# Optimization experiments

Hardware: AMD Instinct MI355X
Metric: run time of the kernel (lower is better)

## Reference

```python
import jax, jax.numpy as jnp
import numpy as np

D = 2048  # input_dimensions (== seq_len, required by the module's math)
H = 8192  # hidden_dimensions
B = 4
S = D


def setup_inputs() -> dict:
    key = jax.random.key(0)
    ks = jax.random.split(key, 13)
    scale_in = 1.0 / np.sqrt(D)
    scale_hid = 1.0 / np.sqrt(H)
    def lin(k, fan_in, fan_out, s):
        return jax.random.normal(k, (fan_in, fan_out), jnp.float32) * s
    inp = {"x": jax.random.normal(ks[0], (B, S, D), jnp.float32)}
    names = ["q", "k", "v"]
    for i, n in enumerate(names):
        inp[f"{n}_w1"] = lin(ks[1 + 4 * i], D, H, scale_in)
        inp[f"{n}_b1"] = jnp.zeros((H,), jnp.float32)
        inp[f"{n}_w2"] = lin(ks[2 + 4 * i], H, D, scale_hid)
        inp[f"{n}_b2"] = jnp.zeros((D,), jnp.float32)
    return inp


def _mlp(x, w1, b1, w2, b2):
    # Linear(D,H) -> ReLU -> Linear(H,D)
    h = jax.nn.relu(jnp.einsum("bsd,dh->bsh", x, w1) + b1)
    return jnp.einsum("bsh,hd->bsd", h, w2) + b2


def reference(x, q_w1, q_b1, q_w2, q_b2, k_w1, k_b1, k_w2, k_b2,
              v_w1, v_b1, v_w2, v_b2):
    Q = _mlp(x, q_w1, q_b1, q_w2, q_b2)
    K = _mlp(x, k_w1, k_b1, k_w2, k_b2)
    V = _mlp(x, v_w1, v_b1, v_w2, v_b2)
    # scores: Q @ K^T  -> [B, S, S]  (no 1/sqrt(d) scaling in original)
    scores = jnp.einsum("bsd,btd->bst", Q, K)
    # nn.Softmax(dim=1): over axis 1 (rows), NOT the usual last axis
    probs = jax.nn.softmax(scores, axis=1)
    # original computes V @ probs (requires S == D)
    out = jnp.einsum("bsd,bdt->bst", V, probs)
    return out
```

## Files before the change

### kernel.cpp

```cpp
#include <hip/hip_runtime.h>
#include <cstdint>
#include <cstddef>

typedef __attribute__((ext_vector_type(8))) short short8;
typedef __attribute__((ext_vector_type(4))) short short4v;
typedef __attribute__((ext_vector_type(4))) float f32x4;
typedef __attribute__((ext_vector_type(4))) int i32x4;

#define DEV __device__ __forceinline__

constexpr int DD = 2048;
constexpr int HHID = 8192;
constexpr int BB = 4;
constexpr int SS = 2048;
constexpr size_t NX = (size_t)BB * SS * DD;
constexpr size_t NW = (size_t)DD * HHID;
constexpr size_t NH = (size_t)BB * SS * HHID;

constexpr size_t OFF_XH  = 0;
constexpr size_t OFF_XA1 = OFF_XH + NX * 2;
constexpr size_t OFF_XA2 = OFF_XA1 + NX;
constexpr size_t OFF_WA1 = OFF_XA2 + NX;
constexpr size_t OFF_WA2 = OFF_WA1 + NW;
constexpr size_t OFF_WHV = OFF_WA1;
constexpr size_t OFF_HH  = OFF_WA2 + NW;
constexpr size_t OFF_HL  = OFF_HH + NH * 2;
constexpr size_t OFF_QKH = OFF_HL + NH * 2;
constexpr size_t OFF_QKL = OFF_QKH + NX * 2;
constexpr size_t OFF_QA1 = OFF_QKL + NX * 2;
constexpr size_t OFF_QA2 = OFF_QA1 + NX;
constexpr size_t OFF_KA1 = OFF_QA2 + NX;
constexpr size_t OFF_KA2 = OFF_KA1 + NX;
constexpr size_t OFF_HA1 = OFF_KA2 + NX;
constexpr size_t OFF_HA2 = OFF_HA1 + NH;
constexpr size_t OFF_V   = OFF_HA2 + NH;
constexpr size_t OFF_XS  = OFF_V + NX * 2;
constexpr size_t OFF_HS  = OFF_XS + 32768;
constexpr size_t OFF_QS  = OFF_HS + 32768;
constexpr size_t OFF_KS  = OFF_QS + 32768;
constexpr size_t OFF_CM  = OFF_KS + 32768;
constexpr size_t WS_TOTAL = OFF_CM + 32768;
constexpr size_t OFF_ST = OFF_HH;
constexpr size_t OFF_PT = OFF_HL;

__device__ __align__(256) unsigned char g_ws[WS_TOTAL];

DEV unsigned char* wsbase(unsigned char* p) { return p ? p : (unsigned char*)g_ws; }
DEV short f2bf(float v) { __bf16 b = (__bf16)v; return __builtin_bit_cast(short, b); }
DEV float bf2f(short s) { return (float)__builtin_bit_cast(__bf16, s); }

template <typename T> DEV void nts(T v, T* p) { __builtin_nontemporal_store(v, p); }
template <typename T> DEV T ntl(const T* p) { return __builtin_nontemporal_load(p); }

DEV void gl16(const short* g, short* l) {
  __builtin_amdgcn_global_load_lds((const __attribute__((address_space(1))) void*)g,
                                   (__attribute__((address_space(3))) void*)l, 16, 0, 0);
}
DEV void gl16b(const signed char* g, signed char* l) {
  __builtin_amdgcn_global_load_lds((const __attribute__((address_space(1))) void*)g,
                                   (__attribute__((address_space(3))) void*)l, 16, 0, 0);
}

DEV void raster2d(int rem, int gx, int grp, int& by, int& bx) {
  const int tpg = grp * gx;
  const int gidx = rem / tpg;
  const int o = rem - gidx * tpg;
  const int r = o / grp;
  by = gidx * grp + (o - r * grp);
  bx = r;
}

__global__ void cast_hi_k(const float* __restrict__ x, unsigned char* wsb,
                          size_t oh, size_t n4) {
  unsigned char* ws = wsbase(wsb);
  short4v* OH = (short4v*)(ws + oh);
  const f32x4* X = (const f32x4*)x;
  for (size_t i = (size_t)blockIdx.x * blockDim.x + threadIdx.x; i < n4;
       i += (size_t)gridDim.x * blockDim.x) {
    const f32x4 v = ntl(&X[i]);
    short4v hs;
#pragma unroll
    for (int e = 0; e < 4; ++e) hs[e] = f2bf(v[e]);
    OH[i] = hs;
  }
}

__launch_bounds__(256)
__global__ void quant_x_k(const float* __restrict__ x, unsigned char* wsb,
                          size_t oa1, size_t oa2, size_t oxs) {
  unsigned char* ws = wsbase(wsb);
  signed char* A1 = (signed char*)(ws + oa1);
  signed char* A2 = (signed char*)(ws + oa2);
  float* XS = (float*)(ws + oxs);
  const int row = blockIdx.x;
  const float* xr = x + (size_t)row * 2048;
  const int tid = threadIdx.x, lane = tid & 63;
  const f32x4 v0 = *(const f32x4*)&xr[tid * 8];
  const f32x4 v1 = *(const f32x4*)&xr[tid * 8 + 4];
  float m = 0.0f;
#pragma unroll
  for (int e = 0; e < 4; ++e) m = fmaxf(m, fmaxf(fabsf(v0[e]), fabsf(v1[e])));
#pragma unroll
  for (int o = 32; o; o >>= 1) m = fmaxf(m, __shfl_xor(m, o));
  __shared__ float rb[4];
  if (lane == 0) rb[tid >> 6] = m;
  __syncthreads();
  m = fmaxf(fmaxf(rb[0], rb[1]), fmaxf(rb[2], rb[3]));
  const float inv = (m > 1e-30f) ? 127.0f / m : 0.0f;
  if (tid == 0) XS[row] = m * (1.0f / 127.0f);
  unsigned int w1a = 0, w1b = 0, w2a = 0, w2b = 0;
#pragma unroll
  for (int e = 0; e < 8; ++e) {
    const float xv = (e < 4) ? v0[e] : v1[e - 4];
    const float q = xv * inv;
    const float a1f = rintf(q);
    int ia2 = (int)rintf((q - a1f) * 256.0f);
    ia2 = ia2 > 127 ? 127 : (ia2 < -127 ? -127 : ia2);
    const unsigned int b1 = (unsigned char)(signed char)(int)a1f;
    const unsigned int b2 = (unsigned char)(signed char)ia2;
    if (e < 4) { w1a |= b1 << (8 * e); w2a |= b2 << (8 * e); }
    else       { w1b |= b1 << (8 * (e - 4)); w2b |= b2 << (8 * (e - 4)); }
  }
  const size_t o = (size_t)row * 2048 + tid * 8;
  *(unsigned int*)&A1[o] = w1a; *(unsigned int*)&A1[o + 4] = w1b;
  *(unsigned int*)&A2[o] = w2a; *(unsigned int*)&A2[o + 4] = w2b;
}

__launch_bounds__(1024)
__global__ void rowquant_k(unsigned char* wsb, size_t hho, size_t hlo,
                           size_t oa1, size_t oa2, size_t oso, int rowlen) {
  unsigned char* ws = wsbase(wsb);
  const int row = blockIdx.x, tid = threadIdx.x, lane = tid & 63, wv = tid >> 6;
  const int nw = blockDim.x >> 6;
  const short8 hi = ntl((const short8*)((const short*)(ws + hho) + (size_t)row * rowlen) + tid);
  const short8 lo = ntl((const short8*)((const short*)(ws + hlo) + (size_t)row * rowlen) + tid);
  float v[8]; float m = 0.0f;
#pragma unroll
  for (int e = 0; e < 8; ++e) {
    v[e] = bf2f(hi[e]) + bf2f(lo[e]);
    m = fmaxf(m, fabsf(v[e]));
  }
#pragma unroll
  for (int o = 32; o; o >>= 1) m = fmaxf(m, __shfl_xor(m, o));
  __shared__ float rb[16];
  if (lane == 0) rb[wv] = m;
  __syncthreads();
  m = rb[0];
  for (int i = 1; i < nw; ++i) m = fmaxf(m, rb[i]);
  const float inv = (m > 1e-30f) ? 127.0f / m : 0.0f;
  if (tid == 0) ((float*)(ws + oso))[row] = m * (1.0f / 127.0f);
  unsigned int w1a = 0, w1b = 0, w2a = 0, w2b = 0;
#pragma unroll
  for (int e = 0; e < 8; ++e) {
    const float q = v[e] * inv;
    const float a1f = rintf(q);
    int ia2 = (int)rintf((q - a1f) * 256.0f);
    ia2 = ia2 > 127 ? 127 : (ia2 < -127 ? -127 : ia2);
    const unsigned int b1 = (unsigned char)(signed char)(int)a1f;
    const unsigned int b2 = (unsigned char)(signed char)ia2;
    if (e < 4) { w1a |= b1 << (8 * e); w2a |= b2 << (8 * e); }
    else       { w1b |= b1 << (8 * (e - 4)); w2b |= b2 << (8 * (e - 4)); }
  }
  const size_t o = (size_t)row * rowlen + tid * 8;
  signed char* A1 = (signed char*)(ws + oa1);
  signed char* A2 = (signed char*)(ws + oa2);
  *(unsigned int*)&A1[o] = w1a; *(unsigned int*)&A1[o + 4] = w1b;
  *(unsigned int*)&A2[o] = w2a; *(unsigned int*)&A2[o + 4] = w2b;
}

__launch_bounds__(256)
__global__ void colmax_k(const float* __restrict__ w, unsigned char* wsb,
                         size_t omax, int R, int C) {
  unsigned char* ws = wsbase(wsb);
  unsigned int* MX = (unsigned int*)(ws + omax);
  const int col = blockIdx.x * 256 + threadIdx.x;
  const int r0 = blockIdx.y * 128;
  float m = 0.0f;
  for (int r = 0; r < 128; ++r) m = fmaxf(m, fabsf(w[(size_t)(r0 + r) * C + col]));
  atomicMax(&MX[col], __float_as_uint(m));
}

__global__ void scalefix_k(unsigned char* wsb, size_t off, int n) {
  unsigned char* ws = wsbase(wsb);
  const int i = blockIdx.x * 256 + threadIdx.x;
  if (i < n) {
    float* p = (float*)(ws + off);
    const unsigned int u = ((const unsigned int*)p)[i];
    p[i] = __uint_as_float(u) * (1.0f / 127.0f);
  }
}

__global__ void transpose_quant_k(const float* __restrict__ src, unsigned char* wsb,
                                  size_t oa1, size_t oa2, size_t osc, int R, int C) {
  __shared__ float t[32][33];
  unsigned char* ws = wsbase(wsb);
  signed char* A1 = (signed char*)(ws + oa1);
  signed char* A2 = (signed char*)(ws + oa2);
  const float* SC = (const float*)(ws + osc);
  const int c0 = blockIdx.x << 5, r0 = blockIdx.y << 5;
  const int x = threadIdx.x, y = threadIdx.y;
#pragma unroll
  for (int i = 0; i < 4; ++i) {
    const int rr = y + (i << 3);
    t[rr][x] = ntl(&src[(size_t)(r0 + rr) * C + c0 + x]);
  }
  __syncthreads();
#pragma unroll
  for (int i = 0; i < 4; ++i) {
    const int oc = y + (i << 3);
    const float v = t[x][oc];
    const float s = SC[c0 + oc];
    const float inv = (s > 1e-38f) ? 1.0f / s : 0.0f;
    const float q = v * inv;
    const float a1f = rintf(q);
    int ia2 = (int)rintf((q - a1f) * 256.0f);
    ia2 = ia2 > 127 ? 127 : (ia2 < -127 ? -127 : ia2);
    const size_t o = (size_t)(c0 + oc) * R + r0 + x;
    A1[o] = (signed char)(int)a1f;
    A2[o] = (signed char)ia2;
  }
}

__global__ void transpose_cast_k(const float* __restrict__ src, unsigned char* wsb,
                                 size_t oh, int R, int C) {
  __shared__ float t[32][33];
  unsigned char* ws = wsbase(wsb);
  short* OH = (short*)(ws + oh);
  const int c0 = blockIdx.x << 5, r0 = blockIdx.y << 5;
  const int x = threadIdx.x, y = threadIdx.y;
#pragma unroll
  for (int i = 0; i < 4; ++i) {
    const int rr = y + (i << 3);
    t[rr][x] = ntl(&src[(size_t)(r0 + rr) * C + c0 + x]);
  }
  __syncthreads();
#pragma unroll
  for (int i = 0; i < 4; ++i) {
    const int oc = y + (i << 3);
    OH[(size_t)(c0 + oc) * R + r0 + x] = f2bf(t[x][oc]);
  }
}

DEV i32x4 mfma_i8(i32x4 a, i32x4 b, i32x4 c) {
  return __builtin_amdgcn_mfma_i32_16x16x64_i8(a, b, c, 0, 0, 0);
}
DEV i32x4 rfi8(const signed char* base, int lstride, int L, int row, int fg) {
  return *(const i32x4*)&base[L * lstride + row * 64 + ((fg ^ ((row >> 1) & 3)) << 4)];
}

template <bool RELU, int STORE>
__launch_bounds__(512, 2)
__global__ void gemm_i8_k(unsigned char* wsb,
                          size_t a1o, size_t a2o, size_t b1o, size_t b2o,
                          size_t aso, size_t bso, const float* __restrict__ bias,
                          size_t o0, size_t o1, int M, int N, int K,
                          int gx, int gxy, int grp) {
  __shared__ alignas(16) signed char lds8[114688];

  unsigned char* ws = wsbase(wsb);
  const int tid = threadIdx.x;
  const int lane = tid & 63;
  const int wave = tid >> 6;
  const int wm = (wave >> 2) << 6;
  const int wn = (wave & 3) << 6;
  const int fr = lane & 15;
  const int fg = lane >> 4;

  const int nwg = gridDim.x;
  const int q8 = nwg >> 3;
  const int id = (blockIdx.x & 7) * q8 + (blockIdx.x >> 3);
  const int bz = id / gxy;
  const int rem = id - bz * gxy;
  int by, bx;
  raster2d(rem, gx, grp, by, bx);
  const int brow = by << 7;
  const int bcol = bx << 8;

  const size_t batchA = (size_t)bz * M * K;
  const size_t batchB = (STORE == 2) ? (size_t)bz * N * K : 0;
  const signed char* Xa1 = (const signed char*)(ws + a1o) + batchA;
  const signed char* Xa2 = (const signed char*)(ws + a2o) + batchA;
  const signed char* Wa1 = (const signed char*)(ws + b1o) + batchB;
  const signed char* Wa2 = (const signed char*)(ws + b2o) + batchB;
  const float* AS = (const float*)(ws + aso) + (size_t)bz * M;
  const float* BS = (const float*)(ws + bso) + ((STORE == 2) ? (size_t)bz * N : 0);

  const int ar = tid >> 2, ac = tid & 3;
  const size_t aOff = (size_t)(brow + ar) * K + ((ac ^ ((ar >> 1) & 3)) << 4);
  size_t bOff[2];
#pragma unroll
  for (int h = 0; h < 2; ++h) {
    const int G = tid + h * 512;
    const int r = G >> 2, c = G & 3;
    bOff[h] = (size_t)(bcol + r) * K + ((c ^ ((r >> 1) & 3)) << 4);
  }

  auto stageA = [&](int slotBase, int tt) {
    const int ko = tt * 64;
    gl16b(Xa1 + aOff + ko, &lds8[slotBase + (tid << 4)]);
    gl16b(Xa2 + aOff + ko, &lds8[slotBase + 8192 + (tid << 4)]);
  };
  auto stageB = [&](int slotBase, int tt) {
    const int ko = tt * 64;
#pragma unroll
    for (int h = 0; h < 2; ++h) {
      gl16b(Wa1 + bOff[h] + ko, &lds8[slotBase + ((tid + h * 512) << 4)]);
      gl16b(Wa2 + bOff[h] + ko, &lds8[slotBase + 16384 + ((tid + h * 512) << 4)]);
    }
  };

  const int nt = K / 64;
  i32x4 I1[4][4] = {};
  i32x4 I2[4][4] = {};

  stageA(0, 0);
  stageB(49152, 0);
  if (nt > 1) { stageA(16384, 1); stageB(49152 + 32768, 1); }
  if (nt > 1) { asm volatile("s_waitcnt vmcnt(6)" ::: "memory"); }
  else        { asm volatile("s_waitcnt vmcnt(0)" ::: "memory"); }
  __builtin_amdgcn_s_barrier();

  for (int t = 0; t < nt; ++t) {
    const signed char* aS = &lds8[(t % 3) * 16384];
    const signed char* bS = &lds8[49152 + (t & 1) * 32768];
    const int sA2 = ((t + 2) % 3) * 16384;
    const int sB2 = 49152 + (t & 1) * 32768;
    const bool pf = (t + 2 < nt);
    i32x4 bf[4][2], af[2][2];

    if (pf) stageA(sA2, t + 2);
#pragma unroll
    for (int j = 0; j < 4; ++j) {
      bf[j][0] = rfi8(bS, 16384, 0, wn + j * 16 + fr, fg);
      bf[j][1] = rfi8(bS, 16384, 1, wn + j * 16 + fr, fg);
    }
#pragma unroll
    for (int i = 0; i < 2; ++i) {
      af[i][0] = rfi8(aS, 8192, 0, wm + i * 16 + fr, fg);
      af[i][1] = rfi8(aS, 8192, 1, wm + i * 16 + fr, fg);
    }
    __builtin_amdgcn_s_setprio(1);
#pragma unroll
    for (int i = 0; i < 2; ++i)
#pragma unroll
      for (int j = 0; j < 4; ++j) {
        I1[i][j] = mfma_i8(af[i][0], bf[j][0], I1[i][j]);
        I2[i][j] = mfma_i8(af[i][0], bf[j][1], I2[i][j]);
        I2[i][j] = mfma_i8(af[i][1], bf[j][0], I2[i][j]);
      }
    __builtin_amdgcn_s_setprio(0);
    __builtin_amdgcn_s_barrier();

    asm volatile("" ::: "memory");
    if (pf) stageB(sB2, t + 2);
#pragma unroll
    for (int i = 0; i < 2; ++i) {
      af[i][0] = rfi8(aS, 8192, 0, wm + (2 + i) * 16 + fr, fg);
      af[i][1] = rfi8(aS, 8192, 1, wm + (2 + i) * 16 + fr, fg);
    }
    __builtin_amdgcn_s_setprio(1);
#pragma unroll
    for (int i = 0; i < 2; ++i)
#pragma unroll
      for (int j = 0; j < 4; ++j) {
        I1[2 + i][j] = mfma_i8(af[i][0], bf[j][0], I1[2 + i][j]);
        I2[2 + i][j] = mfma_i8(af[i][0], bf[j][1], I2[2 + i][j]);
        I2[2 + i][j] = mfma_i8(af[i][1], bf[j][0], I2[2 + i][j]);
      }
    __builtin_amdgcn_s_setprio(0);
    if (pf) { asm volatile("s_waitcnt vmcnt(6)" ::: "memory"); }
    else    { asm volatile("s_waitcnt vmcnt(0)" ::: "memory"); }
    __builtin_amdgcn_s_barrier();
  }

  const int fq4 = fg << 2;
  if constexpr (STORE == 0) {
    short* ldsS = (short*)lds8;
    short* Oh = (short*)(ws + o0);
    short* Ol = (short*)(ws + o1);
#pragma unroll
    for (int rd = 0; rd < 2; ++rd) {
      __builtin_amdgcn_s_barrier();
#pragma unroll
      for (int i = 0; i < 4; ++i) {
        const int rl = wm + i * 16 + fq4;
        const f32x4 sa4 = *(const f32x4*)&AS[brow + rl];
#pragma unroll
        for (int j = 0; j < 4; ++j) {
          const int cl = wn + j * 16 + fr;
          const float sb = BS[bcol + cl];
          const float bv = bias ? bias[bcol + cl] : 0.0f;
#pragma unroll
          for (int e = 0; e < 4; ++e) {
            float u = ((float)I1[i][j][e] + (float)I2[i][j][e] * (1.0f / 256.0f)) *
                          (sa4[e] * sb) + bv;
            if (RELU) u = fmaxf(u, 0.0f);
            short v;
            if (rd == 0) {
              v = f2bf(u);
            } else {
              const short hb = f2bf(u);
              v = f2bf(u - bf2f(hb));
            }
            ldsS[(rl + e) * 264 + cl] = v;
          }
        }
      }
      __builtin_amdgcn_s_barrier();
      short* gout = (rd == 0) ? Oh : Ol;
#pragma unroll
      for (int gi = 0; gi < 8; ++gi) {
        const int g = gi * 512 + tid;
        const int row = g >> 5, cg = g & 31;
        const short8 v = *(const short8*)&ldsS[row * 264 + cg * 8];
        nts(v, (short8*)&gout[(size_t)(brow + row) * N + bcol + cg * 8]);
      }
    }
  } else {
    float* Of = (float*)(ws + o0) + (size_t)bz * M * N;
    float* ldsf = (float*)lds8;
#pragma unroll
    for (int h2 = 0; h2 < 2; ++h2) {
      __builtin_amdgcn_s_barrier();
      if ((wn >> 7) == h2) {
#pragma unroll
        for (int i = 0; i < 4; ++i) {
          const int rl = wm + i * 16 + fq4;
          const f32x4 sa4 = *(const f32x4*)&AS[brow + rl];
#pragma unroll
          for (int j = 0; j < 4; ++j) {
            const int cp = (wn & 127) + j * 16 + fr;
            const float sb = BS[bcol + wn + j * 16 + fr];
            f32x4 u;
#pragma unroll
            for (int e = 0; e < 4; ++e)
              u[e] = ((float)I1[i][j][e] + (float)I2[i][j][e] * (1.0f / 256.0f)) *
                     (sa4[e] * sb);
            *(f32x4*)&ldsf[cp * 132 + rl] = u;
          }
        }
      }
      __builtin_amdgcn_s_barrier();
#pragma unroll
      for (int gi = 0; gi < 8; ++gi) {
        const int g = gi * 512 + tid;
        const int tr = g >> 5, tc4 = (g & 31) << 2;
        const f32x4 v = *(const f32x4*)&ldsf[tr * 132 + tc4];
        nts(v, (f32x4*)&Of[(size_t)(bcol + h2 * 128 + tr) * M + brow + tc4]);
      }
    }
  }
}

constexpr int CH = 8192;

DEV short8 read_frag1(const short* base, int row, int s, int fg) {
  return *(const short8*)&base[row * 64 + ((((s << 2) | fg) ^ (row & 7)) << 3)];
}

DEV f32x4 mfma16(short8 a, short8 b, f32x4 c) {
  return __builtin_amdgcn_mfma_f32_16x16x32_bf16(a, b, c, 0, 0, 0);
}

template <bool RELU, int STORE>
__launch_bounds__(512, 2)
__global__ void gemm8_k(unsigned char* wsb,
                        size_t aoff0, size_t boff0,
                        const float* __restrict__ bias,
                        size_t ooff0, float* __restrict__ optr,
                        int M, int N, int K, int gx, int gxy, int grp) {
  __shared__ alignas(16) short lds[10 * CH];

  unsigned char* ws = wsbase(wsb);
  const int tid = threadIdx.x;
  const int lane = tid & 63;
  const int wave = tid >> 6;
  const int wm = (wave >> 2) << 7;
  const int wn = (wave & 3) << 6;

  const int nwg = gridDim.x;
  const int q8 = nwg >> 3;
  const int id = (blockIdx.x & 7) * q8 + (blockIdx.x >> 3);
  const int bz = id / gxy;
  const int rem = id - bz * gxy;
  int by, bx;
  raster2d(rem, gx, grp, by, bx);
  const int brow = by << 8;
  const int bcol = bx << 8;

  const short* A0 = (const short*)(ws + aoff0) + (size_t)bz * M * K;
  const short* B0g = (const short*)(ws + boff0) + (size_t)bz * N * K;

  size_t aSrc[2][2], bSrc[2][2];
#pragma unroll
  for (int h = 0; h < 2; ++h) {
    const int G = tid + h * 512;
    const int r = G >> 3, c = G & 7;
#pragma unroll
    for (int qq = 0; qq < 2; ++qq) {
      aSrc[qq][h] = (size_t)(brow + qq * 128 + r) * K + (size_t)((c ^ (r & 7)) << 3);
      bSrc[qq][h] = (size_t)(bcol + qq * 128 + r) * K + (size_t)((c ^ (r & 7)) << 3);
    }
  }
  const int ldst0 = tid << 3;

  auto issueA = [&](int slot, int qq, int tt) {
    short* dst = &lds[slot + qq * CH];
    const size_t ka = (size_t)tt * 64;
    gl16(A0 + aSrc[qq][0] + ka, dst + ldst0);
    gl16(A0 + aSrc[qq][1] + ka, dst + ldst0 + CH / 2);
  };
  auto issueB = [&](int slot, int qq, int tt) {
    short* dst = &lds[slot + qq * CH];
    const size_t ka = (size_t)tt * 64;
    gl16(B0g + bSrc[qq][0] + ka, dst + ldst0);
    gl16(B0g + bSrc[qq][1] + ka, dst + ldst0 + CH / 2);
  };

  const int nt = K / 64;
  const int fr = lane & 15;
  const int fg = lane >> 4;

  f32x4 acc[8][4] = {};

  issueA(0, 0, 0); issueA(0, 1, 0);
  issueB(6 * CH, 0, 0); issueB(6 * CH, 1, 0);
  if (nt > 1) {
    issueA(2 * CH, 0, 1); issueA(2 * CH, 1, 1);
    issueB(8 * CH, 0, 1); issueB(8 * CH, 1, 1);
    asm volatile("s_waitcnt vmcnt(8)" ::: "memory");
  } else {
    asm volatile("s_waitcnt vmcnt(0)" ::: "memory");
  }
  __builtin_amdgcn_s_barrier();

  for (int t = 0; t < nt; ++t) {
    const short* aBase = &lds[(t % 3) * (2 * CH)];
    const short* bBase = &lds[6 * CH + (t & 1) * (2 * CH)];
    const int sA2 = ((t + 2) % 3) * (2 * CH);
    const int sB  = 6 * CH + (t & 1) * (2 * CH);
    const bool pf = (t + 2 < nt);
    short8 bfr[4][2], av[4][2];

    if (pf) { issueA(sA2, 0, t + 2); issueA(sA2, 1, t + 2); }
#pragma unroll
    for (int j = 0; j < 4; ++j) {
      bfr[j][0] = read_frag1(bBase, wn + j * 16 + fr, 0, fg);
      bfr[j][1] = read_frag1(bBase, wn + j * 16 + fr, 1, fg);
    }
#pragma unroll
    for (int i = 0; i < 4; ++i) {
      av[i][0] = read_frag1(aBase, wm + i * 16 + fr, 0, fg);
      av[i][1] = read_frag1(aBase, wm + i * 16 + fr, 1, fg);
    }
    __builtin_amdgcn_s_setprio(1);
#pragma unroll
    for (int i = 0; i < 4; ++i)
#pragma unroll
      for (int j = 0; j < 4; ++j) {
        acc[i][j] = mfma16(av[i][0], bfr[j][0], acc[i][j]);
        acc[i][j] = mfma16(av[i][1], bfr[j][1], acc[i][j]);
      }
    __builtin_amdgcn_s_setprio(0);
    __builtin_amdgcn_s_barrier();

    asm volatile("" ::: "memory");
    if (pf) { issueB(sB, 0, t + 2); issueB(sB, 1, t + 2); }
#pragma unroll
    for (int i = 0; i < 4; ++i) {
      av[i][0] = read_frag1(aBase, wm + 64 + i * 16 + fr, 0, fg);
      av[i][1] = read_frag1(aBase, wm + 64 + i * 16 + fr, 1, fg);
    }
    __builtin_amdgcn_s_setprio(1);
#pragma unroll
    for (int i = 0; i < 4; ++i)
#pragma unroll
      for (int j = 0; j < 4; ++j) {
        acc[4 + i][j] = mfma16(av[i][0], bfr[j][0], acc[4 + i][j]);
        acc[4 + i][j] = mfma16(av[i][1], bfr[j][1], acc[4 + i][j]);
      }
    __builtin_amdgcn_s_setprio(0);
    if (pf) {
      asm volatile("s_waitcnt vmcnt(8)" ::: "memory");
    } else {
      asm volatile("s_waitcnt vmcnt(0)" ::: "memory");
    }
    __builtin_amdgcn_s_barrier();
  }

  const int fq4 = (lane >> 4) << 2;
  if constexpr (STORE == 1) {
    short* Oh = (short*)(ws + ooff0);
    __builtin_amdgcn_s_barrier();
#pragma unroll
    for (int i = 0; i < 8; ++i) {
      const int rl = wm + i * 16 + fq4;
#pragma unroll
      for (int j = 0; j < 4; ++j) {
        const int cl = wn + j * 16 + fr;
        const float bv = bias ? bias[bcol + cl] : 0.0f;
#pragma unroll
        for (int e = 0; e < 4; ++e) {
          float u = acc[i][j][e] + bv;
          if (RELU) u = fmaxf(u, 0.0f);
          lds[(rl + e) * 264 + cl] = f2bf(u);
        }
      }
    }
    __builtin_amdgcn_s_barrier();
#pragma unroll
    for (int gi = 0; gi < 16; ++gi) {
      const int g = gi * 512 + tid;
      const int row = g >> 5, cg = g & 31;
      const short8 v = *(const short8*)&lds[row * 264 + cg * 8];
      nts(v, (short8*)&Oh[(size_t)(brow + row) * N + bcol + cg * 8]);
    }
  } else {
    float* Op = optr + (size_t)bz * M * N;
    float* ldsf = (float*)lds;
#pragma unroll
    for (int h = 0; h < 2; ++h) {
      __builtin_amdgcn_s_barrier();
      if ((wm & 128) == (h << 7)) {
#pragma unroll
        for (int i = 0; i < 8; ++i) {
          const int rp = (wm & 127) + i * 16 + fq4;
#pragma unroll
          for (int j = 0; j < 4; ++j) {
            const int cl = wn + j * 16 + fr;
#pragma unroll
            for (int e = 0; e < 4; ++e)
              ldsf[(rp + e) * 258 + cl] = acc[i][j][e];
          }
        }
      }
      __builtin_amdgcn_s_barrier();
#pragma unroll
      for (int gi = 0; gi < 16; ++gi) {
        const int g = gi * 512 + tid;
        const int tr = g >> 6, tc4 = (g & 63) << 2;
        const f32x4 v = *(const f32x4*)&ldsf[tr * 258 + tc4];
        nts(v, (f32x4*)&Op[(size_t)(brow + h * 128 + tr) * N + bcol + tc4]);
      }
    }
  }
}

__launch_bounds__(256)
__global__ void softmax_rows_k(unsigned char* wsb, size_t st, size_t pt) {
  constexpr int S = 2048;
  unsigned char* ws = wsbase(wsb);
  const f32x4* row = (const f32x4*)((const float*)(ws + st) + (size_t)blockIdx.x * S);
  short4v* out = (short4v*)((short*)(ws + pt) + (size_t)blockIdx.x * S);
  const int tid = threadIdx.x, lane = tid & 63, wv = tid >> 6;
  const f32x4 a = ntl(&row[tid]);
  const f32x4 b = ntl(&row[tid + 256]);
  float m = fmaxf(fmaxf(fmaxf(a[0], a[1]), fmaxf(a[2], a[3])),
                  fmaxf(fmaxf(b[0], b[1]), fmaxf(b[2], b[3])));
#pragma unroll
  for (int o = 32; o; o >>= 1) m = fmaxf(m, __shfl_xor(m, o));
  __shared__ float rb[8];
  if (lane == 0) rb[wv] = m;
  __syncthreads();
  m = fmaxf(fmaxf(rb[0], rb[1]), fmaxf(rb[2], rb[3]));
  float e[8];
  float s = 0.0f;
#pragma unroll
  for (int q = 0; q < 4; ++q) { e[q] = expf(a[q] - m); s += e[q]; }
#pragma unroll
  for (int q = 0; q < 4; ++q) { e[4 + q] = expf(b[q] - m); s += e[4 + q]; }
#pragma unroll
  for (int o = 32; o; o >>= 1) s += __shfl_xor(s, o);
  if (lane == 0) rb[4 + wv] = s;
  __syncthreads();
  s = rb[4] + rb[5] + rb[6] + rb[7];
  const float inv = 1.0f / s;
  short4v o1, o2;
#pragma unroll
  for (int q = 0; q < 4; ++q) { o1[q] = f2bf(e[q] * inv); o2[q] = f2bf(e[4 + q] * inv); }
  nts(o1, &out[tid]);
  nts(o2, &out[tid + 256]);
}

extern "C" void kernel_launch(void* const* d_in, const int* in_sizes, int n_in,
                              void* d_out, int out_size, void* d_ws, size_t ws_size,
                              hipStream_t stream) {
  const float* x   = (const float*)d_in[0];
  const float* qw1 = (const float*)d_in[1];
  const float* qb1 = (const float*)d_in[2];
  const float* qw2 = (const float*)d_in[3];
  const float* qb2 = (const float*)d_in[4];
  const float* kw1 = (const float*)d_in[5];
  const float* kb1 = (const float*)d_in[6];
  const float* kw2 = (const float*)d_in[7];
  const float* kb2 = (const float*)d_in[8];
  const float* vw1 = (const float*)d_in[9];
  const float* vb1 = (const float*)d_in[10];
  const float* vw2 = (const float*)d_in[11];
  const float* vb2 = (const float*)d_in[12];
  float* out = (float*)d_out;
  unsigned char* wsb = (ws_size >= WS_TOTAL) ? (unsigned char*)d_ws : nullptr;
  unsigned char* wsr;
  if (wsb) wsr = wsb;
  else { hipError_t e = hipGetSymbolAddress((void**)&wsr, HIP_SYMBOL(g_ws)); (void)e; }

  const int M = BB * SS;
  dim3 blk(512);
  dim3 tb(32, 8);

  quant_x_k<<<8192, 256, 0, stream>>>(x, wsb, OFF_XA1, OFF_XA2, OFF_XS);
  cast_hi_k<<<4096, 256, 0, stream>>>(x, wsb, OFF_XH, NX / 4);

  hipMemsetAsync(wsr + OFF_CM, 0, 32768, stream);
  colmax_k<<<dim3(HHID / 256, DD / 128), 256, 0, stream>>>(qw1, wsb, OFF_CM, DD, HHID);
  scalefix_k<<<32, 256, 0, stream>>>(wsb, OFF_CM, HHID);
  transpose_quant_k<<<dim3(HHID / 32, DD / 32), tb, 0, stream>>>(qw1, wsb, OFF_WA1, OFF_WA2, OFF_CM, DD, HHID);
  gemm_i8_k<true, 0><<<2048, blk, 0, stream>>>(wsb, OFF_XA1, OFF_XA2, OFF_WA1, OFF_WA2,
                                               OFF_XS, OFF_CM, qb1, OFF_HH, OFF_HL,
                                               M, HHID, DD, 32, 2048, 8);
  rowquant_k<<<8192, 1024, 0, stream>>>(wsb, OFF_HH, OFF_HL, OFF_HA1, OFF_HA2, OFF_HS, HHID);
  hipMemsetAsync(wsr + OFF_CM, 0, 32768, stream);
  colmax_k<<<dim3(DD / 256, HHID / 128), 256, 0, stream>>>(qw2, wsb, OFF_CM, HHID, DD);
  scalefix_k<<<8, 256, 0, stream>>>(wsb, OFF_CM, DD);
  transpose_quant_k<<<dim3(DD / 32, HHID / 32), tb, 0, stream>>>(qw2, wsb, OFF_WA1, OFF_WA2, OFF_CM, HHID, DD);
  gemm_i8_k<false, 0><<<512, blk, 0, stream>>>(wsb, OFF_HA1, OFF_HA2, OFF_WA1, OFF_WA2,
                                               OFF_HS, OFF_CM, qb2, OFF_QKH, OFF_QKL,
                                               M, DD, HHID, 8, 512, 8);
  rowquant_k<<<8192, 256, 0, stream>>>(wsb, OFF_QKH, OFF_QKL, OFF_QA1, OFF_QA2, OFF_QS, DD);

  hipMemsetAsync(wsr + OFF_CM, 0, 32768, stream);
  colmax_k<<<dim3(HHID / 256, DD / 128), 256, 0, stream>>>(kw1, wsb, OFF_CM, DD, HHID);
  scalefix_k<<<32, 256, 0, stream>>>(wsb, OFF_CM, HHID);
  transpose_quant_k<<<dim3(HHID / 32, DD / 32), tb, 0, stream>>>(kw1, wsb, OFF_WA1, OFF_WA2, OFF_CM, DD, HHID);
  gemm_i8_k<true, 0><<<2048, blk, 0, stream>>>(wsb, OFF_XA1, OFF_XA2, OFF_WA1, OFF_WA2,
                                               OFF_XS, OFF_CM, kb1, OFF_HH, OFF_HL,
                                               M, HHID, DD, 32, 2048, 8);
  rowquant_k<<<8192, 1024, 0, stream>>>(wsb, OFF_HH, OFF_HL, OFF_HA1, OFF_HA2, OFF_HS, HHID);
  hipMemsetAsync(wsr + OFF_CM, 0, 32768, stream);
  colmax_k<<<dim3(DD / 256, HHID / 128), 256, 0, stream>>>(kw2, wsb, OFF_CM, HHID, DD);
  scalefix_k<<<8, 256, 0, stream>>>(wsb, OFF_CM, DD);
  transpose_quant_k<<<dim3(DD / 32, HHID / 32), tb, 0, stream>>>(kw2, wsb, OFF_WA1, OFF_WA2, OFF_CM, HHID, DD);
  gemm_i8_k<false, 0><<<512, blk, 0, stream>>>(wsb, OFF_HA1, OFF_HA2, OFF_WA1, OFF_WA2,
                                               OFF_HS, OFF_CM, kb2, OFF_QKH, OFF_QKL,
                                               M, DD, HHID, 8, 512, 8);
  rowquant_k<<<8192, 256, 0, stream>>>(wsb, OFF_QKH, OFF_QKL, OFF_KA1, OFF_KA2, OFF_KS, DD);

  transpose_cast_k<<<dim3(HHID / 32, DD / 32), tb, 0, stream>>>(vw1, wsb, OFF_WHV, DD, HHID);
  gemm8_k<true, 1><<<1024, blk, 0, stream>>>(
      wsb, OFF_XH, OFF_WHV, vb1, OFF_HH, nullptr, M, HHID, DD, 32, 1024, 4);
  transpose_cast_k<<<dim3(DD / 32, HHID / 32), tb, 0, stream>>>(vw2, wsb, OFF_WHV, HHID, DD);
  gemm8_k<false, 1><<<256, blk, 0, stream>>>(
      wsb, OFF_HH, OFF_WHV, vb2, OFF_V, nullptr, M, DD, HHID, 8, 256, 4);

  gemm_i8_k<false, 2><<<512, blk, 0, stream>>>(wsb, OFF_QA1, OFF_QA2, OFF_KA1, OFF_KA2,
                                               OFF_QS, OFF_KS, nullptr, OFF_ST, 0,
                                               SS, SS, DD, 8, 128, 8);

  softmax_rows_k<<<BB * SS, 256, 0, stream>>>(wsb, OFF_ST, OFF_PT);

  gemm8_k<false, 3><<<256, blk, 0, stream>>>(
      wsb, OFF_V, OFF_PT, nullptr, 0, out, SS, SS, DD, 8, 64, 4);
}
```

Measured before the change: 2.672 ms.

## Fuse int8 row quantization into GEMM epilogue with per-tile scales and rescale pass

The GEMM epilogue now quantizes its output directly to the two-level int8 format, using a per-tile row max, and writes per-tile scales. It no longer writes a bf16 hi/lo pair that a separate row-quantization kernel reread. A light rescale kernel then computes each row's global max and requantizes only the tiles whose scale differs. This cuts the large bf16 intermediate traffic for the hidden and Q/K activations, at the cost of a second rounding step that can lose some precision. Barriers in the epilogues were also switched from raw s_barrier to __syncthreads.

Result: no change. 2.696 ms (+0.9%).

```diff
diff --git a/kernel.cpp b/kernel.cpp
--- a/kernel.cpp
+++ b/kernel.cpp
@@ -24,24 +24,23 @@
 constexpr size_t OFF_WA2 = OFF_WA1 + NW;
 constexpr size_t OFF_WHV = OFF_WA1;
 constexpr size_t OFF_HH  = OFF_WA2 + NW;
-constexpr size_t OFF_HL  = OFF_HH + NH * 2;
-constexpr size_t OFF_QKH = OFF_HL + NH * 2;
-constexpr size_t OFF_QKL = OFF_QKH + NX * 2;
-constexpr size_t OFF_QA1 = OFF_QKL + NX * 2;
+constexpr size_t OFF_PT  = OFF_HH + NH * 2;
+constexpr size_t OFF_HA1 = OFF_PT + NX * 2;
+constexpr size_t OFF_HA2 = OFF_HA1 + NH;
+constexpr size_t OFF_QA1 = OFF_HA2 + NH;
 constexpr size_t OFF_QA2 = OFF_QA1 + NX;
 constexpr size_t OFF_KA1 = OFF_QA2 + NX;
 constexpr size_t OFF_KA2 = OFF_KA1 + NX;
-constexpr size_t OFF_HA1 = OFF_KA2 + NX;
-constexpr size_t OFF_HA2 = OFF_HA1 + NH;
-constexpr size_t OFF_V   = OFF_HA2 + NH;
+constexpr size_t OFF_V   = OFF_KA2 + NX;
 constexpr size_t OFF_XS  = OFF_V + NX * 2;
 constexpr size_t OFF_HS  = OFF_XS + 32768;
 constexpr size_t OFF_QS  = OFF_HS + 32768;
 constexpr size_t OFF_KS  = OFF_QS + 32768;
 constexpr size_t OFF_CM  = OFF_KS + 32768;
-constexpr size_t WS_TOTAL = OFF_CM + 32768;
+constexpr size_t OFF_TSH = OFF_CM + 32768;
+constexpr size_t OFF_TSQ = OFF_TSH + 8192 * 32 * 4;
+constexpr size_t WS_TOTAL = OFF_TSQ + 8192 * 8 * 4;
 constexpr size_t OFF_ST = OFF_HH;
-constexpr size_t OFF_PT = OFF_HL;
 
 __device__ __align__(256) unsigned char g_ws[WS_TOTAL];
 
@@ -126,46 +125,46 @@
   *(unsigned int*)&A2[o] = w2a; *(unsigned int*)&A2[o + 4] = w2b;
 }
 
-__launch_bounds__(1024)
-__global__ void rowquant_k(unsigned char* wsb, size_t hho, size_t hlo,
-                           size_t oa1, size_t oa2, size_t oso, int rowlen) {
-  unsigned char* ws = wsbase(wsb);
-  const int row = blockIdx.x, tid = threadIdx.x, lane = tid & 63, wv = tid >> 6;
-  const int nw = blockDim.x >> 6;
-  const short8 hi = ntl((const short8*)((const short*)(ws + hho) + (size_t)row * rowlen) + tid);
-  const short8 lo = ntl((const short8*)((const short*)(ws + hlo) + (size_t)row * rowlen) + tid);
-  float v[8]; float m = 0.0f;
-#pragma unroll
-  for (int e = 0; e < 8; ++e) {
-    v[e] = bf2f(hi[e]) + bf2f(lo[e]);
-    m = fmaxf(m, fabsf(v[e]));
-  }
-#pragma unroll
-  for (int o = 32; o; o >>= 1) m = fmaxf(m, __shfl_xor(m, o));
-  __shared__ float rb[16];
-  if (lane == 0) rb[wv] = m;
+__launch_bounds__(256)
+__global__ void rescale_k(unsigned char* wsb, size_t a1o, size_t a2o,
+                          size_t tso, size_t so, int rowlen) {
+  unsigned char* ws = wsbase(wsb);
+  const int row = blockIdx.x, tid = threadIdx.x;
+  const int nblk = rowlen >> 8;
+  const float* TS = (const float*)(ws + tso) + (size_t)row * nblk;
+  __shared__ float ratio[32];
+  __shared__ float srow_sh;
+  if (tid == 0) {
+    float m = 0.0f;
+    for (int i = 0; i < nblk; ++i) m = fmaxf(m, TS[i]);
+    srow_sh = m;
+    ((float*)(ws + so))[row] = m;
+  }
   __syncthreads();
-  m = rb[0];
-  for (int i = 1; i < nw; ++i) m = fmaxf(m, rb[i]);
-  const float inv = (m > 1e-30f) ? 127.0f / m : 0.0f;
-  if (tid == 0) ((float*)(ws + oso))[row] = m * (1.0f / 127.0f);
-  unsigned int w1a = 0, w1b = 0, w2a = 0, w2b = 0;
-#pragma unroll
-  for (int e = 0; e < 8; ++e) {
-    const float q = v[e] * inv;
-    const float a1f = rintf(q);
-    int ia2 = (int)rintf((q - a1f) * 256.0f);
-    ia2 = ia2 > 127 ? 127 : (ia2 < -127 ? -127 : ia2);
-    const unsigned int b1 = (unsigned char)(signed char)(int)a1f;
-    const unsigned int b2 = (unsigned char)(signed char)ia2;
-    if (e < 4) { w1a |= b1 << (8 * e); w2a |= b2 << (8 * e); }
-    else       { w1b |= b1 << (8 * (e - 4)); w2b |= b2 << (8 * (e - 4)); }
-  }
-  const size_t o = (size_t)row * rowlen + tid * 8;
-  signed char* A1 = (signed char*)(ws + oa1);
-  signed char* A2 = (signed char*)(ws + oa2);
-  *(unsigned int*)&A1[o] = w1a; *(unsigned int*)&A1[o + 4] = w1b;
-  *(unsigned int*)&A2[o] = w2a; *(unsigned int*)&A2[o + 4] = w2b;
+  const float srow = srow_sh;
+  if (tid < nblk) ratio[tid] = (srow > 0.0f) ? TS[tid] / srow : 0.0f;
+  __syncthreads();
+  unsigned int* A1 = (unsigned int*)((signed char*)(ws + a1o) + (size_t)row * rowlen);
+  unsigned int* A2 = (unsigned int*)((signed char*)(ws + a2o) + (size_t)row * rowlen);
+  const int nu = rowlen >> 2;
+  for (int u = tid; u < nu; u += 256) {
+    const float r = ratio[u >> 6];
+    if (r == 1.0f) continue;
+    const unsigned int w1 = A1[u], w2 = A2[u];
+    unsigned int o1 = 0, o2 = 0;
+#pragma unroll
+    for (int e = 0; e < 4; ++e) {
+      const float a1 = (float)(signed char)(w1 >> (8 * e));
+      const float a2 = (float)(signed char)(w2 >> (8 * e));
+      const float f = r * (a1 + a2 * (1.0f / 256.0f));
+      const float n1 = rintf(f);
+      int i2 = (int)rintf((f - n1) * 256.0f);
+      i2 = i2 > 127 ? 127 : (i2 < -127 ? -127 : i2);
+      o1 |= ((unsigned int)(unsigned char)(signed char)(int)n1) << (8 * e);
+      o2 |= ((unsigned int)(unsigned char)(signed char)i2) << (8 * e);
+    }
+    A1[u] = o1; A2[u] = o2;
+  }
 }
 
 __launch_bounds__(256)
@@ -253,7 +252,7 @@
 __global__ void gemm_i8_k(unsigned char* wsb,
                           size_t a1o, size_t a2o, size_t b1o, size_t b2o,
                           size_t aso, size_t bso, const float* __restrict__ bias,
-                          size_t o0, size_t o1, int M, int N, int K,
+                          size_t o0, size_t o1, size_t o2, int M, int N, int K,
                           int gx, int gxy, int grp) {
   __shared__ alignas(16) signed char lds8[114688];
 
@@ -374,13 +373,54 @@
   }
 
   const int fq4 = fg << 2;
-  if constexpr (STORE == 0) {
-    short* ldsS = (short*)lds8;
-    short* Oh = (short*)(ws + o0);
-    short* Ol = (short*)(ws + o1);
+  if constexpr (STORE == 4) {
+    signed char* O1 = (signed char*)(ws + o0);
+    signed char* O2 = (signed char*)(ws + o1);
+    float* TS = (float*)(ws + o2);
+    const int nblk = N >> 8;
+    unsigned int* rmaxU = (unsigned int*)&lds8[36864];
+    float* rmaxF = (float*)rmaxU;
+    if (tid < 128) rmaxU[tid] = 0;
+    __syncthreads();
+    float sbj[4], bvj[4];
+#pragma unroll
+    for (int j = 0; j < 4; ++j) {
+      const int cl = wn + j * 16 + fr;
+      sbj[j] = BS[bcol + cl];
+      bvj[j] = bias ? bias[bcol + cl] : 0.0f;
+    }
+#pragma unroll
+    for (int i = 0; i < 4; ++i) {
+      const int rl = wm + i * 16 + fq4;
+      const f32x4 sa4 = *(const f32x4*)&AS[brow + rl];
+      float mx[4] = {0.0f, 0.0f, 0.0f, 0.0f};
+#pragma unroll
+      for (int j = 0; j < 4; ++j)
+#pragma unroll
+        for (int e = 0; e < 4; ++e) {
+          float u = ((float)I1[i][j][e] + (float)I2[i][j][e] * (1.0f / 256.0f)) *
+                        (sa4[e] * sbj[j]) + bvj[j];
+          if (RELU) u = fmaxf(u, 0.0f);
+          mx[e] = fmaxf(mx[e], fabsf(u));
+        }
+#pragma unroll
+      for (int e = 0; e < 4; ++e)
+        atomicMax(&rmaxU[rl + e], __float_as_uint(mx[e]));
+    }
+    __syncthreads();
+    if (tid < 128)
+      TS[(size_t)(brow + tid) * nblk + (bcol >> 8)] = rmaxF[tid] * (1.0f / 127.0f);
+    float invv[4][4];
+#pragma unroll
+    for (int i = 0; i < 4; ++i)
+#pragma unroll
+      for (int e = 0; e < 4; ++e) {
+        const float rm = rmaxF[wm + i * 16 + fq4 + e];
+        invv[i][e] = (rm > 1e-30f) ? 127.0f / rm : 0.0f;
+      }
 #pragma unroll
     for (int rd = 0; rd < 2; ++rd) {
-      __builtin_amdgcn_s_barrier();
+      __syncthreads();
 #pragma unroll
       for (int i = 0; i < 4; ++i) {
         const int rl = wm + i * 16 + fq4;
@@ -388,32 +428,33 @@
 #pragma unroll
         for (int j = 0; j < 4; ++j) {
           const int cl = wn + j * 16 + fr;
-          const float sb = BS[bcol + cl];
-          const float bv = bias ? bias[bcol + cl] : 0.0f;
 #pragma unroll
           for (int e = 0; e < 4; ++e) {
             float u = ((float)I1[i][j][e] + (float)I2[i][j][e] * (1.0f / 256.0f)) *
-                          (sa4[e] * sb) + bv;
+                          (sa4[e] * sbj[j]) + bvj[j];
             if (RELU) u = fmaxf(u, 0.0f);
-            short v;
+            const float q = u * invv[i][e];
+            const float n1 = rintf(q);
+            signed char vq;
             if (rd == 0) {
-              v = f2bf(u);
+              vq = (signed char)(int)n1;
             } else {
-              const short hb = f2bf(u);
-              v = f2bf(u - bf2f(hb));
+              int i2 = (int)rintf((q - n1) * 256.0f);
+              i2 = i2 > 127 ? 127 : (i2 < -127 ? -127 : i2);
+              vq = (signed char)i2;
             }
-            ldsS[(rl + e) * 264 + cl] = v;
+            lds8[(rl + e) * 272 + cl] = vq;
           }
         }
       }
-      __builtin_amdgcn_s_barrier();
-      short* gout = (rd == 0) ? Oh : Ol;
-#pragma unroll
-      for (int gi = 0; gi < 8; ++gi) {
+      __syncthreads();
+      signed char* Og = rd ? O2 : O1;
+#pragma unroll
+      for (int gi = 0; gi < 4; ++gi) {
         const int g = gi * 512 + tid;
-        const int row = g >> 5, cg = g & 31;
-        const short8 v = *(const short8*)&ldsS[row * 264 + cg * 8];
-        nts(v, (short8*)&gout[(size_t)(brow + row) * N + bcol + cg * 8]);
+        const int row = g >> 4, c16 = (g & 15) << 4;
+        const f32x4 v = *(const f32x4*)&lds8[row * 272 + c16];
+        nts(v, (f32x4*)&Og[(size_t)(brow + row) * N + bcol + c16]);
       }
     }
   } else {
@@ -421,7 +462,7 @@
     float* ldsf = (float*)lds8;
 #pragma unroll
     for (int h2 = 0; h2 < 2; ++h2) {
-      __builtin_amdgcn_s_barrier();
+      __syncthreads();
       if ((wn >> 7) == h2) {
 #pragma unroll
         for (int i = 0; i < 4; ++i) {
@@ -440,7 +481,7 @@
           }
         }
       }
-      __builtin_amdgcn_s_barrier();
+      __syncthreads();
 #pragma unroll
       for (int gi = 0; gi < 8; ++gi) {
         const int g = gi * 512 + tid;
@@ -591,7 +632,7 @@
   const int fq4 = (lane >> 4) << 2;
   if constexpr (STORE == 1) {
     short* Oh = (short*)(ws + ooff0);
-    __builtin_amdgcn_s_barrier();
+    __syncthreads();
 #pragma unroll
     for (int i = 0; i < 8; ++i) {
       const int rl = wm + i * 16 + fq4;
@@ -607,7 +648,7 @@
         }
       }
     }
-    __builtin_amdgcn_s_barrier();
+    __syncthreads();
 #pragma unroll
     for (int gi = 0; gi < 16; ++gi) {
       const int g = gi * 512 + tid;
@@ -620,7 +661,7 @@
     float* ldsf = (float*)lds;
 #pragma unroll
     for (int h = 0; h < 2; ++h) {
-      __builtin_amdgcn_s_barrier();
+      __syncthreads();
       if ((wm & 128) == (h << 7)) {
 #pragma unroll
         for (int i = 0; i < 8; ++i) {
@@ -634,7 +675,7 @@
           }
         }
       }
-      __builtin_amdgcn_s_barrier();
+      __syncthreads();
 #pragma unroll
       for (int gi = 0; gi < 16; ++gi) {
         const int g = gi * 512 + tid;
@@ -715,35 +756,35 @@
   colmax_k<<<dim3(HHID / 256, DD / 128), 256, 0, stream>>>(qw1, wsb, OFF_CM, DD, HHID);
   scalefix_k<<<32, 256, 0, stream>>>(wsb, OFF_CM, HHID);
   transpose_quant_k<<<dim3(HHID / 32, DD / 32), tb, 0, stream>>>(qw1, wsb, OFF_WA1, OFF_WA2, OFF_CM, DD, HHID);
-  gemm_i8_k<true, 0><<<2048, blk, 0, stream>>>(wsb, OFF_XA1, OFF_XA2, OFF_WA1, OFF_WA2,
-                                               OFF_XS, OFF_CM, qb1, OFF_HH, OFF_HL,
+  gemm_i8_k<true, 4><<<2048, blk, 0, stream>>>(wsb, OFF_XA1, OFF_XA2, OFF_WA1, OFF_WA2,
+                                               OFF_XS, OFF_CM, qb1, OFF_HA1, OFF_HA2, OFF_TSH,
                                                M, HHID, DD, 32, 2048, 8);
-  rowquant_k<<<8192, 1024, 0, stream>>>(wsb, OFF_HH, OFF_HL, OFF_HA1, OFF_HA2, OFF_HS, HHID);
+  rescale_k<<<8192, 256, 0, stream>>>(wsb, OFF_HA1, OFF_HA2, OFF_TSH, OFF_HS, HHID);
   hipMemsetAsync(wsr + OFF_CM, 0, 32768, stream);
   colmax_k<<<dim3(DD / 256, HHID / 128), 256, 0, stream>>>(qw2, wsb, OFF_CM, HHID, DD);
   scalefix_k<<<8, 256, 0, stream>>>(wsb, OFF_CM, DD);
   transpose_quant_k<<<dim3(DD / 32, HHID / 32), tb, 0, stream>>>(qw2, wsb, OFF_WA1, OFF_WA2, OFF_CM, HHID, DD);
-  gemm_i8_k<false, 0><<<512, blk, 0, stream>>>(wsb, OFF_HA1, OFF_HA2, OFF_WA1, OFF_WA2,
-                                               OFF_HS, OFF_CM, qb2, OFF_QKH, OFF_QKL,
+  gemm_i8_k<false, 4><<<512, blk, 0, stream>>>(wsb, OFF_HA1, OFF_HA2, OFF_WA1, OFF_WA2,
+                                               OFF_HS, OFF_CM, qb2, OFF_QA1, OFF_QA2, OFF_TSQ,
                                                M, DD, HHID, 8, 512, 8);
-  rowquant_k<<<8192, 256, 0, stream>>>(wsb, OFF_QKH, OFF_QKL, OFF_QA1, OFF_QA2, OFF_QS, DD);
+  rescale_k<<<8192, 256, 0, stream>>>(wsb, OFF_QA1, OFF_QA2, OFF_TSQ, OFF_QS, DD);
 
   hipMemsetAsync(wsr + OFF_CM, 0, 32768, stream);
   colmax_k<<<dim3(HHID / 256, DD / 128), 256, 0, stream>>>(kw1, wsb, OFF_CM, DD, HHID);
   scalefix_k<<<32, 256, 0, stream>>>(wsb, OFF_CM, HHID);
   transpose_quant_k<<<dim3(HHID / 32, DD / 32), tb, 0, stream>>>(kw1, wsb, OFF_WA1, OFF_WA2, OFF_CM, DD, HHID);
-  gemm_i8_k<true, 0><<<2048, blk, 0, stream>>>(wsb, OFF_XA1, OFF_XA2, OFF_WA1, OFF_WA2,
-                                               OFF_XS, OFF_CM, kb1, OFF_HH, OFF_HL,
+  gemm_i8_k<true, 4><<<2048, blk, 0, stream>>>(wsb, OFF_XA1, OFF_XA2, OFF_WA1, OFF_WA2,
+                                               OFF_XS, OFF_CM, kb1, OFF_HA1, OFF_HA2, OFF_TSH,
                                                M, HHID, DD, 32, 2048, 8);
-  rowquant_k<<<8192, 1024, 0, stream>>>(wsb, OFF_HH, OFF_HL, OFF_HA1, OFF_HA2, OFF_HS, HHID);
+  rescale_k<<<8192, 256, 0, stream>>>(wsb, OFF_HA1, OFF_HA2, OFF_TSH, OFF_HS, HHID);
   hipMemsetAsync(wsr + OFF_CM, 0, 32768, stream);
   colmax_k<<<dim3(DD / 256, HHID / 128), 256, 0, stream>>>(kw2, wsb, OFF_CM, HHID, DD);
   scalefix_k<<<8, 256, 0, stream>>>(wsb, OFF_CM, DD);
   transpose_quant_k<<<dim3(DD / 32, HHID / 32), tb, 0, stream>>>(kw2, wsb, OFF_WA1, OFF_WA2, OFF_CM, HHID, DD);
-  gemm_i8_k<false, 0><<<512, blk, 0, stream>>>(wsb, OFF_HA1, OFF_HA2, OFF_WA1, OFF_WA2,
-                                               OFF_HS, OFF_CM, kb2, OFF_QKH, OFF_QKL,
+  gemm_i8_k<false, 4><<<512, blk, 0, stream>>>(wsb, OFF_HA1, OFF_HA2, OFF_WA1, OFF_WA2,
+                                               OFF_HS, OFF_CM, kb2, OFF_KA1, OFF_KA2, OFF_TSQ,
                                                M, DD, HHID, 8, 512, 8);
-  rowquant_k<<<8192, 256, 0, stream>>>(wsb, OFF_QKH, OFF_QKL, OFF_KA1, OFF_KA2, OFF_KS, DD);
+  rescale_k<<<8192, 256, 0, stream>>>(wsb, OFF_KA1, OFF_KA2, OFF_TSQ, OFF_KS, DD);
 
   transpose_cast_k<<<dim3(HHID / 32, DD / 32), tb, 0, stream>>>(vw1, wsb, OFF_WHV, DD, HHID);
   gemm8_k<true, 1><<<1024, blk, 0, stream>>>(
@@ -753,7 +794,7 @@
       wsb, OFF_HH, OFF_WHV, vb2, OFF_V, nullptr, M, DD, HHID, 8, 256, 4);
 
   gemm_i8_k<false, 2><<<512, blk, 0, stream>>>(wsb, OFF_QA1, OFF_QA2, OFF_KA1, OFF_KA2,
-                                               OFF_QS, OFF_KS, nullptr, OFF_ST, 0,
+                                               OFF_QS, OFF_KS, nullptr, OFF_ST, 0, 0,
                                                SS, SS, DD, 8, 128, 8);
 
   softmax_rows_k<<<BB * SS, 256, 0, stream>>>(wsb, OFF_ST, OFF_PT);
```
